# Kernel tuning notes

Hardware: AMD Instinct MI355X
Metric: run time of the kernel (lower is better)

## Reference

```python
import jax, jax.numpy as jnp
import numpy as np

# Dimensions (match init_kwargs / input_specs)
B, T, HW, K, J = 8192, 64, 8, 64, 3
FILT_LEN = 8
NEG_SLOPE = 0.001
DWT_OUT_LEN = 84  # lo(14) + hi1(35) + hi2(21) + hi3(14)

# db4 analysis filters (pywt dec_lo / dec_hi)
DB4_LO = np.array([-0.010597401784997278, 0.032883011666982945,
                   0.030841381835986965, -0.18703481171888114,
                   -0.02798376941698385, 0.6308807679295904,
                   0.7148465705525415, 0.23037781330885523], dtype=np.float32)
DB4_HI = np.array([-0.23037781330885523, 0.7148465705525415,
                   -0.6308807679295904, -0.02798376941698385,
                   0.18703481171888114, 0.030841381835986965,
                   0.032883011666982945, -0.010597401784997278], dtype=np.float32)
# pytorch_wavelets stores filters reversed and uses conv1d (cross-correlation)
_H = jnp.asarray(np.ascontiguousarray(np.stack([DB4_LO[::-1], DB4_HI[::-1]])[:, None, :]))  # [2,1,8]


def _afb1d(x):
    # Single-level analysis filter bank along last axis, reflect padding, stride 2.
    # x: [N, n] -> (lo, hi) each [N, floor((n+7)/2)]
    n = x.shape[-1]
    out = (n + FILT_LEN - 1) // 2
    p = 2 * (out - 1) - n + FILT_LEN
    xp = jnp.pad(x, ((0, 0), (p // 2, (p + 1) // 2)), mode='reflect')
    y = jax.lax.conv_general_dilated(xp[:, None, :], _H, (2,), 'VALID')  # [N,2,out]
    return y[:, 0], y[:, 1]


def _dwt(x):
    # J-level DWT; concat [lo_J, hi_1, hi_2, ..., hi_J] along last axis -> [N, 84]
    lo, his = x, []
    for _ in range(J):
        lo, hi = _afb1d(lo)
        his.append(hi)
    return jnp.concatenate([lo] + his, axis=-1)


def setup_inputs() -> dict:
    key = jax.random.key(0)
    k1, k2 = jax.random.split(key)
    x = jax.random.normal(k1, (B, 1, T, HW, HW), dtype=jnp.float32)
    fan_in = DWT_OUT_LEN * HW * HW
    conv_w = jax.random.normal(k2, (K, DWT_OUT_LEN, HW, HW), dtype=jnp.float32) / np.sqrt(fan_in).astype(np.float32)
    conv_b = jnp.zeros((K,), dtype=jnp.float32)
    return {"x": x, "conv_w": conv_w, "conv_b": conv_b}


def reference(x, conv_w, conv_b):
    # x: [B,1,T,H,W]; time_interval=1 and spatial_maxpool_size=1 -> no-ops.
    b = x.shape[0]
    # DWT along time for every (batch, spatial) signal, fully batched.
    sig = x[:, 0].transpose(0, 2, 3, 1).reshape(b * HW * HW, T)  # [B*H*W, T]
    coeffs = _dwt(sig).reshape(b, HW, HW, DWT_OUT_LEN)           # [B,H,W,84]
    # Conv3d with kernel covering the full (84,8,8) volume == one GEMM per output channel.
    feat = jnp.einsum('bhwt,kthw->bk', coeffs, conv_w) + conv_b  # [B,K]
    # Dropout3d in eval mode is identity; LeakyReLU then flatten -> [B, K]
    return jnp.where(feat >= 0, feat, NEG_SLOPE * feat)
```

## Files before the change

kernel.cpp:

```cpp
#include <hip/hip_runtime.h>

typedef __attribute__((ext_vector_type(4))) float floatx4;
typedef __attribute__((ext_vector_type(8))) short shortx8;

__device__ __constant__ float DLO[8] = {
    -0.010597401784997278f, 0.032883011666982945f,
     0.030841381835986965f, -0.18703481171888114f,
    -0.02798376941698385f,  0.6308807679295904f,
     0.7148465705525415f,   0.23037781330885523f};
__device__ __constant__ float DHI[8] = {
    -0.23037781330885523f,  0.7148465705525415f,
    -0.6308807679295904f,  -0.02798376941698385f,
     0.18703481171888114f,  0.030841381835986965f,
     0.032883011666982945f, -0.010597401784997278f};

__device__ __forceinline__ unsigned short f2bf_rne(float f) {
  unsigned u = __builtin_bit_cast(unsigned, f);
  unsigned r = (u + 0x7FFFu + ((u >> 16) & 1u)) >> 16;
  return (unsigned short)r;
}

template <int N, int OUT>
__device__ __forceinline__ void afb(const float* x, float* lo, float* hi) {
#pragma unroll
  for (int m = 0; m < OUT; ++m) {
    float aL = 0.f, aH = 0.f;
#pragma unroll
    for (int i = 0; i < 8; ++i) {
      int s = 2 * m + 1 - i;
      s = (s < 0) ? -s : s;
      s = (s >= N) ? (2 * N - 2 - s) : s;
      float v = x[s];
      aL = fmaf(DLO[i], v, aL);
      aH = fmaf(DHI[i], v, aH);
    }
    lo[m] = aL; hi[m] = aH;
  }
}

__global__ __launch_bounds__(256) void build_w2_fused(
    const float* __restrict__ cw, unsigned short* __restrict__ W2) {
  __shared__ float Ml[84 * 64];
  __shared__ float Cl[84 * 64];
  const int k = blockIdx.x;
  const int tid = threadIdx.x;

  if (tid < 64) {
    const int i = tid;
    float sig[64];
#pragma unroll
    for (int t = 0; t < 64; ++t) sig[t] = (t == i) ? 1.f : 0.f;
    float lo1[35], hi1[35], lo2[21], hi2[21], lo3[14], hi3[14];
    afb<64, 35>(sig, lo1, hi1);
    afb<35, 21>(lo1, lo2, hi2);
    afb<21, 14>(lo2, lo3, hi3);
#pragma unroll
    for (int t = 0; t < 14; ++t) Ml[t * 64 + i] = lo3[t];
#pragma unroll
    for (int t = 0; t < 35; ++t) Ml[(14 + t) * 64 + i] = hi1[t];
#pragma unroll
    for (int t = 0; t < 21; ++t) Ml[(49 + t) * 64 + i] = hi2[t];
#pragma unroll
    for (int t = 0; t < 14; ++t) Ml[(70 + t) * 64 + i] = hi3[t];
  }
  const float* cwk = cw + (size_t)k * (84 * 64);
  for (int idx = tid; idx < 84 * 64; idx += 256) Cl[idx] = cwk[idx];
  __syncthreads();

  const int tp  = blockIdx.y * 16 + (tid >> 4);
  const int hw0 = (tid & 15) * 4;
  float a0 = 0.f, a1 = 0.f, a2 = 0.f, a3 = 0.f;
#pragma unroll 4
  for (int t = 0; t < 84; ++t) {
    const float mv = Ml[t * 64 + tp];
    const float4 cv = *(const float4*)&Cl[t * 64 + hw0];
    a0 = fmaf(mv, cv.x, a0);
    a1 = fmaf(mv, cv.y, a1);
    a2 = fmaf(mv, cv.z, a2);
    a3 = fmaf(mv, cv.w, a3);
  }
  uint2 pk;
  pk.x = (unsigned)f2bf_rne(a0) | ((unsigned)f2bf_rne(a1) << 16);
  pk.y = (unsigned)f2bf_rne(a2) | ((unsigned)f2bf_rne(a3) << 16);
  *(uint2*)(W2 + (size_t)k * 4096 + tp * 64 + hw0) = pk;
}


#define NCH 16

__global__ __launch_bounds__(512) void gemm_kernel(
    const float* __restrict__ A, const unsigned short* __restrict__ W2,
    const float* __restrict__ bias, float* __restrict__ out) {
  __shared__ floatx4 red[8 * 4 * 64];

  const int tid  = threadIdx.x;
  const int lane = tid & 63;
  const int wave = tid >> 6;
  const int frow = lane & 15;
  const int fk   = (lane >> 4) * 8;
  const int m0   = blockIdx.x * 16;
  const int k0   = wave * (NCH * 32);

  const float* aptr = A + (size_t)(m0 + frow) * 4096 + k0 + fk;
  const unsigned short* bptr = W2 + (size_t)frow * 4096 + k0 + fk;

  floatx4 acc0 = {0.f, 0.f, 0.f, 0.f};
  floatx4 acc1 = acc0, acc2 = acc0, acc3 = acc0;

  float4 alo_0, ahi_0, alo_1, ahi_1;
  uint4  bq_0[4], bq_1[4];
  alo_0 = *(const float4*)(aptr + 0);
  ahi_0 = *(const float4*)(aptr + 4);
  alo_1 = *(const float4*)(aptr + 32);
  ahi_1 = *(const float4*)(aptr + 36);
#pragma unroll
  for (int nt = 0; nt < 4; ++nt) {
    bq_0[nt] = *(const uint4*)(bptr + nt * 65536);
    bq_1[nt] = *(const uint4*)(bptr + nt * 65536 + 32);
  }

#define STEP(S, C)                                                           \
  do {                                                                       \
    shortx8 af;                                                              \
    af[0] = (short)f2bf_rne(alo_##S.x); af[1] = (short)f2bf_rne(alo_##S.y);  \
    af[2] = (short)f2bf_rne(alo_##S.z); af[3] = (short)f2bf_rne(alo_##S.w);  \
    af[4] = (short)f2bf_rne(ahi_##S.x); af[5] = (short)f2bf_rne(ahi_##S.y);  \
    af[6] = (short)f2bf_rne(ahi_##S.z); af[7] = (short)f2bf_rne(ahi_##S.w);  \
    acc0 = __builtin_amdgcn_mfma_f32_16x16x32_bf16(                          \
        af, __builtin_bit_cast(shortx8, bq_##S[0]), acc0, 0, 0, 0);          \
    acc1 = __builtin_amdgcn_mfma_f32_16x16x32_bf16(                          \
        af, __builtin_bit_cast(shortx8, bq_##S[1]), acc1, 0, 0, 0);          \
    acc2 = __builtin_amdgcn_mfma_f32_16x16x32_bf16(                          \
        af, __builtin_bit_cast(shortx8, bq_##S[2]), acc2, 0, 0, 0);          \
    acc3 = __builtin_amdgcn_mfma_f32_16x16x32_bf16(                          \
        af, __builtin_bit_cast(shortx8, bq_##S[3]), acc3, 0, 0, 0);          \
    if ((C) + 2 < NCH) {                                                     \
      const int cc = ((C) + 2) * 32;                                         \
      alo_##S = *(const float4*)(aptr + cc);                                 \
      ahi_##S = *(const float4*)(aptr + cc + 4);                             \
      _Pragma("unroll")                                                      \
      for (int nt = 0; nt < 4; ++nt)                                         \
        bq_##S[nt] = *(const uint4*)(bptr + nt * 65536 + cc);                \
    }                                                                        \
  } while (0)

#pragma unroll 2
  for (int c = 0; c < NCH; c += 2) {
    STEP(0, c);
    STEP(1, c + 1);
  }
#undef STEP

  red[(wave * 4 + 0) * 64 + lane] = acc0;
  red[(wave * 4 + 1) * 64 + lane] = acc1;
  red[(wave * 4 + 2) * 64 + lane] = acc2;
  red[(wave * 4 + 3) * 64 + lane] = acc3;
  __syncthreads();

  const float* redf = (const float*)red;
  for (int o = tid; o < 1024; o += 512) {
    const int m  = o >> 6;
    const int n  = o & 63;
    const int l  = ((m >> 2) << 4) | (n & 15);
    const int r  = m & 3;
    const int nt = n >> 4;
    float s = bias[n];
#pragma unroll
    for (int w = 0; w < 8; ++w)
      s += redf[(((w * 4 + nt) * 64 + l) << 2) | r];
    out[(size_t)(m0 + m) * 64 + n] = (s >= 0.f) ? s : 1.0e-3f * s;
  }
}

extern "C" void kernel_launch(void* const* d_in, const int* in_sizes, int n_in,
                              void* d_out, int out_size, void* d_ws, size_t ws_size,
                              hipStream_t stream) {
  const float* x      = (const float*)d_in[0];
  const float* conv_w = (const float*)d_in[1];
  const float* conv_b = (const float*)d_in[2];
  float* out = (float*)d_out;

  unsigned short* W2 = (unsigned short*)d_ws;

  build_w2_fused<<<dim3(64, 4), 256, 0, stream>>>(conv_w, W2);
  gemm_kernel<<<512, 512, 0, stream>>>(x, W2, conv_b, out);
}
```

Before: 212.3 us.

## Stage W2 K-slice in LDS and split-K GEMM with separate reduce kernel

The GEMM is reorganised so each block covers 128 rows and a quarter of K (1024), with the 64x1024 bf16 weight slice staged once into padded LDS and shared by 8 waves, instead of every wave reading weights from global memory. Partial sums go to a workspace, and a new reduce kernel adds the four K-slices, applies bias and LeakyReLU. This removes redundant global weight traffic and the in-block cross-wave reduction. The cost is an extra kernel launch, a partial-sum round trip to memory, and only 256 blocks with large LDS use, which may limit occupancy.

```diff
diff --git a/kernel.cpp b/kernel.cpp
--- a/kernel.cpp
+++ b/kernel.cpp
@@ -85,91 +85,116 @@
   *(uint2*)(W2 + (size_t)k * 4096 + tp * 64 + hw0) = pk;
 }
 
-
-#define NCH 16
+#define LDB 1032
 
 __global__ __launch_bounds__(512) void gemm_kernel(
     const float* __restrict__ A, const unsigned short* __restrict__ W2,
-    const float* __restrict__ bias, float* __restrict__ out) {
-  __shared__ floatx4 red[8 * 4 * 64];
+    float* __restrict__ part) {
+  __shared__ alignas(16) unsigned short Bs[64 * LDB];
 
   const int tid  = threadIdx.x;
   const int lane = tid & 63;
   const int wave = tid >> 6;
   const int frow = lane & 15;
   const int fk   = (lane >> 4) * 8;
-  const int m0   = blockIdx.x * 16;
-  const int k0   = wave * (NCH * 32);
-
-  const float* aptr = A + (size_t)(m0 + frow) * 4096 + k0 + fk;
-  const unsigned short* bptr = W2 + (size_t)frow * 4096 + k0 + fk;
+  const int kb   = blockIdx.y;
+  const int m0   = blockIdx.x * 128 + wave * 16;
+  const int kbase = kb * 1024;
+
+  const float* aptr = A + (size_t)(m0 + frow) * 4096 + kbase + fk;
+
+  float4 al0 = *(const float4*)(aptr + 0),   ah0 = *(const float4*)(aptr + 4);
+  float4 al1 = *(const float4*)(aptr + 32),  ah1 = *(const float4*)(aptr + 36);
+  float4 al2 = *(const float4*)(aptr + 64),  ah2 = *(const float4*)(aptr + 68);
+  float4 al3 = *(const float4*)(aptr + 96),  ah3 = *(const float4*)(aptr + 100);
+
+  {
+    const unsigned short* wsrc = W2 + kbase;
+#pragma unroll
+    for (int j = 0; j < 16; ++j) {
+      const int e = (tid + j * 512) * 8;
+      const int r = e >> 10, cc = e & 1023;
+      const uint4 v = *(const uint4*)(wsrc + (size_t)r * 4096 + cc);
+      *(uint4*)&Bs[r * LDB + cc] = v;
+    }
+  }
+  __asm__ __volatile__("s_waitcnt lgkmcnt(0)\n\ts_barrier" ::: "memory");
 
   floatx4 acc0 = {0.f, 0.f, 0.f, 0.f};
   floatx4 acc1 = acc0, acc2 = acc0, acc3 = acc0;
 
-  float4 alo_0, ahi_0, alo_1, ahi_1;
-  uint4  bq_0[4], bq_1[4];
-  alo_0 = *(const float4*)(aptr + 0);
-  ahi_0 = *(const float4*)(aptr + 4);
-  alo_1 = *(const float4*)(aptr + 32);
-  ahi_1 = *(const float4*)(aptr + 36);
-#pragma unroll
-  for (int nt = 0; nt < 4; ++nt) {
-    bq_0[nt] = *(const uint4*)(bptr + nt * 65536);
-    bq_1[nt] = *(const uint4*)(bptr + nt * 65536 + 32);
-  }
-
-#define STEP(S, C)                                                           \
+  const unsigned short* bsr = &Bs[frow * LDB + fk];
+
+#define CORE(SL, C)                                                          \
+    shortx8 af;                                                              \
+    af[0] = (short)f2bf_rne(al##SL.x); af[1] = (short)f2bf_rne(al##SL.y);    \
+    af[2] = (short)f2bf_rne(al##SL.z); af[3] = (short)f2bf_rne(al##SL.w);    \
+    af[4] = (short)f2bf_rne(ah##SL.x); af[5] = (short)f2bf_rne(ah##SL.y);    \
+    af[6] = (short)f2bf_rne(ah##SL.z); af[7] = (short)f2bf_rne(ah##SL.w);    \
+    {                                                                        \
+      shortx8 bf0 = *(const shortx8*)(bsr + 0 * 16 * LDB + (C) * 32);        \
+      shortx8 bf1 = *(const shortx8*)(bsr + 1 * 16 * LDB + (C) * 32);        \
+      shortx8 bf2 = *(const shortx8*)(bsr + 2 * 16 * LDB + (C) * 32);        \
+      shortx8 bf3 = *(const shortx8*)(bsr + 3 * 16 * LDB + (C) * 32);        \
+      acc0 = __builtin_amdgcn_mfma_f32_16x16x32_bf16(af, bf0, acc0, 0, 0, 0);\
+      acc1 = __builtin_amdgcn_mfma_f32_16x16x32_bf16(af, bf1, acc1, 0, 0, 0);\
+      acc2 = __builtin_amdgcn_mfma_f32_16x16x32_bf16(af, bf2, acc2, 0, 0, 0);\
+      acc3 = __builtin_amdgcn_mfma_f32_16x16x32_bf16(af, bf3, acc3, 0, 0, 0);\
+    }
+
+#define STEPP(SL, C)                                                         \
   do {                                                                       \
-    shortx8 af;                                                              \
-    af[0] = (short)f2bf_rne(alo_##S.x); af[1] = (short)f2bf_rne(alo_##S.y);  \
-    af[2] = (short)f2bf_rne(alo_##S.z); af[3] = (short)f2bf_rne(alo_##S.w);  \
-    af[4] = (short)f2bf_rne(ahi_##S.x); af[5] = (short)f2bf_rne(ahi_##S.y);  \
-    af[6] = (short)f2bf_rne(ahi_##S.z); af[7] = (short)f2bf_rne(ahi_##S.w);  \
-    acc0 = __builtin_amdgcn_mfma_f32_16x16x32_bf16(                          \
-        af, __builtin_bit_cast(shortx8, bq_##S[0]), acc0, 0, 0, 0);          \
-    acc1 = __builtin_amdgcn_mfma_f32_16x16x32_bf16(                          \
-        af, __builtin_bit_cast(shortx8, bq_##S[1]), acc1, 0, 0, 0);          \
-    acc2 = __builtin_amdgcn_mfma_f32_16x16x32_bf16(                          \
-        af, __builtin_bit_cast(shortx8, bq_##S[2]), acc2, 0, 0, 0);          \
-    acc3 = __builtin_amdgcn_mfma_f32_16x16x32_bf16(                          \
-        af, __builtin_bit_cast(shortx8, bq_##S[3]), acc3, 0, 0, 0);          \
-    if ((C) + 2 < NCH) {                                                     \
-      const int cc = ((C) + 2) * 32;                                         \
-      alo_##S = *(const float4*)(aptr + cc);                                 \
-      ahi_##S = *(const float4*)(aptr + cc + 4);                             \
-      _Pragma("unroll")                                                      \
-      for (int nt = 0; nt < 4; ++nt)                                         \
-        bq_##S[nt] = *(const uint4*)(bptr + nt * 65536 + cc);                \
-    }                                                                        \
+    CORE(SL, C)                                                              \
+    al##SL = *(const float4*)(aptr + ((C) + 4) * 32);                        \
+    ah##SL = *(const float4*)(aptr + ((C) + 4) * 32 + 4);                    \
   } while (0)
 
-#pragma unroll 2
-  for (int c = 0; c < NCH; c += 2) {
-    STEP(0, c);
-    STEP(1, c + 1);
-  }
-#undef STEP
-
-  red[(wave * 4 + 0) * 64 + lane] = acc0;
-  red[(wave * 4 + 1) * 64 + lane] = acc1;
-  red[(wave * 4 + 2) * 64 + lane] = acc2;
-  red[(wave * 4 + 3) * 64 + lane] = acc3;
-  __syncthreads();
-
-  const float* redf = (const float*)red;
-  for (int o = tid; o < 1024; o += 512) {
-    const int m  = o >> 6;
-    const int n  = o & 63;
-    const int l  = ((m >> 2) << 4) | (n & 15);
-    const int r  = m & 3;
-    const int nt = n >> 4;
-    float s = bias[n];
-#pragma unroll
-    for (int w = 0; w < 8; ++w)
-      s += redf[(((w * 4 + nt) * 64 + l) << 2) | r];
-    out[(size_t)(m0 + m) * 64 + n] = (s >= 0.f) ? s : 1.0e-3f * s;
-  }
+#define STEPN(SL, C) do { CORE(SL, C) } while (0)
+
+  for (int c = 0; c < 28; c += 4) {
+    STEPP(0, c);
+    STEPP(1, c + 1);
+    STEPP(2, c + 2);
+    STEPP(3, c + 3);
+  }
+  STEPN(0, 28);
+  STEPN(1, 29);
+  STEPN(2, 30);
+  STEPN(3, 31);
+#undef STEPP
+#undef STEPN
+#undef CORE
+
+  float* pp = part + (((size_t)kb * 8192 + m0) << 6);
+  const int prow = (lane >> 4) * 4;
+  const int pcol = lane & 15;
+#define ST(NT, ACC)                                                          \
+  _Pragma("unroll")                                                          \
+  for (int r = 0; r < 4; ++r)                                                \
+    pp[(prow + r) * 64 + (NT) * 16 + pcol] = ACC[r];
+  ST(0, acc0) ST(1, acc1) ST(2, acc2) ST(3, acc3)
+#undef ST
+}
+
+__global__ __launch_bounds__(256) void reduce_kernel(
+    const float* __restrict__ part, const float* __restrict__ bias,
+    float* __restrict__ out) {
+  const int o = (blockIdx.x * 256 + threadIdx.x) * 4;
+  const float4 s0 = *(const float4*)(part + o);
+  const float4 s1 = *(const float4*)(part + 524288 + o);
+  const float4 s2 = *(const float4*)(part + 1048576 + o);
+  const float4 s3 = *(const float4*)(part + 1572864 + o);
+  const float4 bv = *(const float4*)(bias + (o & 63));
+  float4 r;
+  r.x = s0.x + s1.x + s2.x + s3.x + bv.x;
+  r.y = s0.y + s1.y + s2.y + s3.y + bv.y;
+  r.z = s0.z + s1.z + s2.z + s3.z + bv.z;
+  r.w = s0.w + s1.w + s2.w + s3.w + bv.w;
+  r.x = (r.x >= 0.f) ? r.x : 1.0e-3f * r.x;
+  r.y = (r.y >= 0.f) ? r.y : 1.0e-3f * r.y;
+  r.z = (r.z >= 0.f) ? r.z : 1.0e-3f * r.z;
+  r.w = (r.w >= 0.f) ? r.w : 1.0e-3f * r.w;
+  *(float4*)(out + o) = r;
 }
 
 extern "C" void kernel_launch(void* const* d_in, const int* in_sizes, int n_in,
@@ -181,7 +206,9 @@
   float* out = (float*)d_out;
 
   unsigned short* W2 = (unsigned short*)d_ws;
+  float* part = (float*)((char*)d_ws + (1 << 20));
 
   build_w2_fused<<<dim3(64, 4), 256, 0, stream>>>(conv_w, W2);
-  gemm_kernel<<<512, 512, 0, stream>>>(x, W2, conv_b, out);
-}
+  gemm_kernel<<<dim3(64, 4), 512, 0, stream>>>(x, W2, part);
+  reduce_kernel<<<512, 256, 0, stream>>>(part, conv_b, out);
+}
```

Result: no change. 213.7 us (+0.6%).
